# Kernel tuning notes

Hardware: AMD Instinct MI355X
Metric: run time of the kernel (lower is better)

Reference implementation:

```python
import jax, jax.numpy as jnp
import numpy as np

B, N, E = 16, 2048, 1024
G, V = 2, 320
D = E // G
TAU = 2.0


def setup_inputs() -> dict:
    key = jax.random.key(0)
    k1, k2, k3, k4 = jax.random.split(key, 4)
    x = jax.random.normal(k1, (B, N, E), dtype=jnp.float32)
    u = jax.random.uniform(k2, (B, N, G, V), dtype=jnp.float32)
    W = jax.random.normal(k3, (E, G * V), dtype=jnp.float32) * 0.02
    b = jnp.zeros((G * V,), dtype=jnp.float32)
    codebook = jax.random.normal(k4, (G, V, D), dtype=jnp.float32)
    return {"x": x, "u": u, "W": W, "b": b, "codebook": codebook}


def reference(x, u, W, b, codebook):
    Bx, Nx, Ex = x.shape
    Gx, Vx, Dx = codebook.shape
    # linear projection -> per-group logits [B,N,G,V]
    h = (jnp.einsum('bne,ef->bnf', x, W) + b).reshape(Bx, Nx, Gx, Vx)
    # gumbel noise from uniform samples (clamped away from 0/1)
    eps = 1e-7
    g = -jnp.log(-jnp.log(u * (1.0 - 2.0 * eps) + eps))
    soft = jax.nn.softmax((h + g) / TAU, axis=-1)
    # hard one-hot with straight-through estimator (matches torch hard=True)
    idx = jnp.argmax(soft, axis=-1)
    hard = jax.nn.one_hot(idx, Vx, dtype=soft.dtype)
    y = hard - jax.lax.stop_gradient(soft) + soft  # [B,N,G,V]
    # select code vectors: equivalent to broadcast-mul + sum over V
    code_vector = jnp.einsum('bngv,gvd->bngd', y, codebook).reshape(Bx, Nx, Gx * Dx)
    # codebook usage entropy: sum one-hots over time, softmax over V per group
    p = jax.nn.softmax(jnp.sum(y, axis=1), axis=-1)  # [B,G,V]
    entropy = -jnp.sum(p * jnp.log(p + 1e-8)) / (Gx * Vx)
    return code_vector, entropy
```

## Files before the change

kernel.cpp:

```cpp
#include <hip/hip_runtime.h>

namespace {

constexpr int Bsz = 16, Nsz = 2048, Esz = 1024, Gsz = 2, Vsz = 320, Dsz = 512;
constexpr int Msz = Bsz * Nsz;
constexpr int Fsz = Gsz * Vsz;
constexpr int BM = 128, BN = 128, BK = 32;
constexpr int NKC = Esz / 32;

typedef __attribute__((ext_vector_type(8))) short bf16x8;
typedef __attribute__((ext_vector_type(4))) float f32x4;
typedef unsigned int u32;
typedef unsigned short u16;

__device__ __forceinline__ void load_lds16(const void* g, void* l) {
  __builtin_amdgcn_global_load_lds(
      (const __attribute__((address_space(1))) u32*)g,
      (__attribute__((address_space(3))) u32*)l, 16, 0, 0);
}

__device__ __forceinline__ ushort f2bf(float f) {
  union { float f; unsigned u; } v; v.f = f;
  unsigned r = (v.u + 0x7FFFu + ((v.u >> 16) & 1u)) >> 16;
  return (ushort)r;
}
__device__ __forceinline__ float bf2f(ushort h) {
  union { unsigned u; float f; } v; v.u = ((unsigned)h) << 16;
  return v.f;
}

__device__ __forceinline__ float gumb_precise(float uu) {
  const float C0 = 1.0f - 2.0f * 1e-7f;
  float up = uu * C0;
  up = up + 1e-7f;
  return -logf(-logf(up));
}
__device__ __forceinline__ float gumb_fast(float uu) {
  const float C0 = 1.0f - 2.0f * 1e-7f;
  const float up = fmaf(uu, C0, 1e-7f);
  const float d = 1.0f - up;
  const float ypoly =
      d * fmaf(d, fmaf(d, fmaf(d, fmaf(d, 0.2f, 0.25f), 0.33333334f), 0.5f), 1.0f);
  const float yfast = -__logf(up);
  const float y = (up >= 0.84f) ? ypoly : yfast;
  return -__logf(y);
}

struct Top2 { float v1, v2; int i1, i2; };
__device__ __forceinline__ void t2_feed(Top2& t, float z, int f) {
  if (z > t.v1 || (z == t.v1 && f < t.i1)) {
    t.v2 = t.v1; t.i2 = t.i1; t.v1 = z; t.i1 = f;
  } else if (z > t.v2 || (z == t.v2 && f < t.i2)) {
    t.v2 = z; t.i2 = f;
  }
}
__device__ __forceinline__ void t2_merge(Top2& t, float ov1, int oi1, float ov2,
                                         int oi2) {
  if (ov1 > t.v1 || (ov1 == t.v1 && oi1 < t.i1)) {
    const bool keep = (t.v1 > ov2) || (t.v1 == ov2 && t.i1 < oi2);
    t.v2 = keep ? t.v1 : ov2; t.i2 = keep ? t.i1 : oi2;
    t.v1 = ov1; t.i1 = oi1;
  } else if (ov1 > t.v2 || (ov1 == t.v2 && oi1 < t.i2)) {
    t.v2 = ov1; t.i2 = oi1;
  }
}

__device__ __forceinline__ uint2 pack_hi_trunc(float4 a) {
  uint2 r;
  r.x = (__float_as_uint(a.x) >> 16) | (__float_as_uint(a.y) & 0xffff0000u);
  r.y = (__float_as_uint(a.z) >> 16) | (__float_as_uint(a.w) & 0xffff0000u);
  return r;
}
__device__ __forceinline__ float4 resid_trunc(float4 a) {
  float4 r;
  r.x = a.x - __uint_as_float(__float_as_uint(a.x) & 0xffff0000u);
  r.y = a.y - __uint_as_float(__float_as_uint(a.y) & 0xffff0000u);
  r.z = a.z - __uint_as_float(__float_as_uint(a.z) & 0xffff0000u);
  r.w = a.w - __uint_as_float(__float_as_uint(a.w) & 0xffff0000u);
  return r;
}


__global__ __launch_bounds__(256) void k_prep(const float* __restrict__ W,
                                              u16* __restrict__ wt) {
  const int tid = threadIdx.x;
  const int l = tid & 63;
  const int blob = blockIdx.x * 4 + (tid >> 6);
  const int fb = blob >> 5, kc = blob & 31;
  const int f = fb * 16 + (l & 15);
  const int k0 = kc * 32 + (l >> 4) * 8;
  ushort hh[8], ll[8];
#pragma unroll
  for (int j = 0; j < 8; ++j) {
    const float v = W[(size_t)(k0 + j) * Fsz + f];
    hh[j] = f2bf(v);
    ll[j] = f2bf(v - bf2f(hh[j]));
  }
  uint4 qh, ql;
  qh.x = hh[0] | ((u32)hh[1] << 16); qh.y = hh[2] | ((u32)hh[3] << 16);
  qh.z = hh[4] | ((u32)hh[5] << 16); qh.w = hh[6] | ((u32)hh[7] << 16);
  ql.x = ll[0] | ((u32)ll[1] << 16); ql.y = ll[2] | ((u32)ll[3] << 16);
  ql.z = ll[4] | ((u32)ll[5] << 16); ql.w = ll[6] | ((u32)ll[7] << 16);
  *(uint4*)(wt + ((size_t)blob * 2 + 0) * 512 + l * 8) = qh;
  *(uint4*)(wt + ((size_t)blob * 2 + 1) * 512 + l * 8) = ql;
}

__global__ __launch_bounds__(256) void k_prepx(const float* __restrict__ x,
                                               u16* __restrict__ xt) {
  const int tid = threadIdx.x;
  const int l = tid & 63;
  const int blob = blockIdx.x * 4 + (tid >> 6);
  const int mb = blob >> 5, kc = blob & 31;
  const size_t row = (size_t)mb * 16 + (l & 15);
  const int k0 = kc * 32 + (l >> 4) * 8;
  const float4 a0 = *(const float4*)(x + row * Esz + k0);
  const float4 a1 = *(const float4*)(x + row * Esz + k0 + 4);
  const uint2 h0 = pack_hi_trunc(a0), h1 = pack_hi_trunc(a1);
  const uint2 l0 = pack_hi_trunc(resid_trunc(a0));
  const uint2 l1 = pack_hi_trunc(resid_trunc(a1));
  uint4 qh, ql;
  qh.x = h0.x; qh.y = h0.y; qh.z = h1.x; qh.w = h1.y;
  ql.x = l0.x; ql.y = l0.y; ql.z = l1.x; ql.w = l1.y;
  *(uint4*)(xt + ((size_t)blob * 2 + 0) * 512 + l * 8) = qh;
  *(uint4*)(xt + ((size_t)blob * 2 + 1) * 512 + l * 8) = ql;
}

__global__ __launch_bounds__(256, 4) void k_gemm(
    const float* __restrict__ u, const float* __restrict__ bias,
    const u16* __restrict__ xt, const u16* __restrict__ wt,
    float4* __restrict__ partial) {
  __shared__ __align__(16) u16 sm[12288];
  u16* As = sm;
  u16* Bs = sm + 8192;

  const int tid = threadIdx.x;
  const int bid = blockIdx.x;
  const int tile = (bid & 7) * 320 + (bid >> 3);
  const int mt = tile / 10, nt = tile - mt * 10;
  const int m0 = mt * BM;
  const int n0 = nt * 64;

  const int lane = tid & 63, w = tid >> 6;
  const int lrow = lane & 15, quad = lane >> 4;

  f32x4 acc[2][4];
#pragma unroll
  for (int i = 0; i < 2; ++i)
#pragma unroll
    for (int j = 0; j < 4; ++j) acc[i][j] = (f32x4){0.f, 0.f, 0.f, 0.f};

  const u16* src0[6];
  u16* dst0[6];
#pragma unroll
  for (int i = 0; i < 6; ++i) {
    const int cc = w + 4 * i;
    const int isA = (cc < 16) ? 1 : 0;
    const int c = isA ? cc : (cc - 16);
    const int gb = (isA ? (m0 >> 4) : (n0 >> 4)) + (c >> 1);
    const int p = c & 1;
    src0[i] = (isA ? xt : wt) + ((size_t)gb * NKC * 2 + p) * 512 + lane * 8;
    dst0[i] = (isA ? As : Bs) + c * 512;
  }

#pragma unroll
  for (int i = 0; i < 6; ++i) load_lds16(src0[i], dst0[i]);

  for (int kc = 0; kc < NKC; ++kc) {
    __syncthreads();
    bf16x8 ah[2], al[2], bh[4], bl[4];
#pragma unroll
    for (int rt = 0; rt < 2; ++rt) {
      const int blk = w * 2 + rt;
      ah[rt] = *(const bf16x8*)(As + (blk * 2 + 0) * 512 + lane * 8);
      al[rt] = *(const bf16x8*)(As + (blk * 2 + 1) * 512 + lane * 8);
    }
#pragma unroll
    for (int ct = 0; ct < 4; ++ct) {
      bh[ct] = *(const bf16x8*)(Bs + (ct * 2 + 0) * 512 + lane * 8);
      bl[ct] = *(const bf16x8*)(Bs + (ct * 2 + 1) * 512 + lane * 8);
    }
    __syncthreads();
    if (kc + 1 < NKC) {
      const size_t off = (size_t)(kc + 1) * 1024;
#pragma unroll
      for (int i = 0; i < 6; ++i) load_lds16(src0[i] + off, dst0[i]);
    }
    __builtin_amdgcn_sched_barrier(0);
#pragma unroll
    for (int ct = 0; ct < 4; ++ct)
#pragma unroll
      for (int rt = 0; rt < 2; ++rt) {
        acc[rt][ct] = __builtin_amdgcn_mfma_f32_16x16x32_bf16(al[rt], bh[ct], acc[rt][ct], 0, 0, 0);
        acc[rt][ct] = __builtin_amdgcn_mfma_f32_16x16x32_bf16(ah[rt], bl[ct], acc[rt][ct], 0, 0, 0);
        acc[rt][ct] = __builtin_amdgcn_mfma_f32_16x16x32_bf16(ah[rt], bh[ct], acc[rt][ct], 0, 0, 0);
      }
  }

  const int pcol = nt;
#pragma unroll
  for (int rt = 0; rt < 2; ++rt) {
#pragma unroll
    for (int rg = 0; rg < 4; ++rg) {
      const int row = w * 32 + rt * 16 + quad * 4 + rg;
      const size_t m = (size_t)(m0 + row);
      Top2 t; t.v1 = -3.4e38f; t.v2 = -3.4e38f; t.i1 = 1 << 30; t.i2 = 1 << 30;
#pragma unroll
      for (int ct = 0; ct < 4; ++ct) {
        const int f = n0 + ct * 16 + lrow;
        const float z = acc[rt][ct][rg] + bias[f] + gumb_fast(u[m * 640 + f]);
        t2_feed(t, z, f);
      }
#pragma unroll
      for (int off = 1; off < 16; off <<= 1) {
        const float ov1 = __shfl_xor(t.v1, off, 16);
        const int oi1 = __shfl_xor(t.i1, off, 16);
        const float ov2 = __shfl_xor(t.v2, off, 16);
        const int oi2 = __shfl_xor(t.i2, off, 16);
        t2_merge(t, ov1, oi1, ov2, oi2);
      }
      if (lrow == 0) {
        float4 o;
        o.x = t.v1; o.y = __int_as_float(t.i1);
        o.z = t.v2; o.w = __int_as_float(t.i2);
        partial[m * 10 + pcol] = o;
      }
    }
  }
}

__global__ __launch_bounds__(256) void k_select(
    const float4* __restrict__ partial, const float* __restrict__ x,
    const float* __restrict__ W, const float* __restrict__ bias,
    const float* __restrict__ u, int2* __restrict__ idx_out,
    int* __restrict__ counts) {
  const int tid = threadIdx.x;
  const size_t m = (size_t)blockIdx.x * 256 + tid;
  int vsel[2];
#pragma unroll
  for (int g = 0; g < 2; ++g) {
    Top2 t; t.v1 = -3.4e38f; t.v2 = -3.4e38f; t.i1 = 1 << 30; t.i2 = 1 << 30;
#pragma unroll
    for (int p = 0; p < 5; ++p) {
      const float4 q = partial[m * 10 + g * 5 + p];
      t2_merge(t, q.x, __float_as_int(q.y), q.z, __float_as_int(q.w));
    }
    int i1 = t.i1;
    if (t.v1 - t.v2 < 1e-3f) {
      const int i2 = t.i2;
      const float* xp = x + m * Esz;
      float h1 = 0.f, h2 = 0.f;
      for (int k = 0; k < Esz; ++k) {
        const float xv = xp[k];
        h1 = fmaf(xv, W[(size_t)k * Fsz + i1], h1);
        h2 = fmaf(xv, W[(size_t)k * Fsz + i2], h2);
      }
      const float z1 = h1 + bias[i1] + gumb_precise(u[m * 640 + i1]);
      const float z2 = h2 + bias[i2] + gumb_precise(u[m * 640 + i2]);
      if (z2 > z1 || (z2 == z1 && i2 < i1)) i1 = i2;
    }
    const int v = i1 - g * Vsz;
    vsel[g] = v;
    const int b = (int)(m >> 11);
    atomicAdd(&counts[(b * Gsz + g) * Vsz + v], 1);
  }
  int2 r; r.x = vsel[0]; r.y = vsel[1];
  idx_out[m] = r;
}

__global__ __launch_bounds__(256) void k_gather(const int2* __restrict__ idx,
                                                const float* __restrict__ cb,
                                                float* __restrict__ out) {
  __shared__ int2 sidx[32];
  const int tid = threadIdx.x;
  const size_t mbase = (size_t)blockIdx.x * 32;
  if (tid < 32) sidx[tid] = idx[mbase + tid];
  __syncthreads();
  const int gq = tid >> 7, dq = tid & 127;
  for (int it = 0; it < 32; ++it) {
    const int2 p = sidx[it];
    const int v = gq ? p.y : p.x;
    const float4 cv =
        *(const float4*)(cb + ((size_t)(gq * Vsz + v)) * Dsz + dq * 4);
    *(float4*)(out + (mbase + it) * (size_t)(Gsz * Dsz) + tid * 4) = cv;
  }
}


__global__ __launch_bounds__(256) void k_prep_fb(const float* __restrict__ W,
                                                 u16* __restrict__ wt_h,
                                                 u16* __restrict__ wt_l) {
  const int f = blockIdx.x;
  const int k0 = threadIdx.x * 4;
  float v[4];
#pragma unroll
  for (int i = 0; i < 4; ++i) v[i] = W[(size_t)(k0 + i) * Fsz + f];
  ushort4 hh, ll;
  hh.x = f2bf(v[0]); ll.x = f2bf(v[0] - bf2f(hh.x));
  hh.y = f2bf(v[1]); ll.y = f2bf(v[1] - bf2f(hh.y));
  hh.z = f2bf(v[2]); ll.z = f2bf(v[2] - bf2f(hh.z));
  hh.w = f2bf(v[3]); ll.w = f2bf(v[3] - bf2f(hh.w));
  *(ushort4*)(wt_h + (size_t)f * Esz + k0) = hh;
  *(ushort4*)(wt_l + (size_t)f * Esz + k0) = ll;
}

__global__ __launch_bounds__(256) void k_gemm_fb(
    const float* __restrict__ x, const float* __restrict__ u,
    const float* __restrict__ bias, const u16* __restrict__ wth,
    const u16* __restrict__ wtl, float4* __restrict__ partial) {
  __shared__ __align__(16) u16 sm[16384];
  u16* xs_h = sm;
  u16* xs_l = sm + 4096;
  u16* bs_h = sm + 8192;
  u16* bs_l = sm + 12288;

  const int tid = threadIdx.x;
  const int n0 = blockIdx.x * BN;
  const int m0 = blockIdx.y * BM;
  const int lane = tid & 63, w = tid >> 6;
  const int wr = w >> 1, wc = w & 1;
  const int lrow = lane & 15, quad = lane >> 4;

  f32x4 acc[4][4];
#pragma unroll
  for (int i = 0; i < 4; ++i)
#pragma unroll
    for (int j = 0; j < 4; ++j) acc[i][j] = (f32x4){0.f, 0.f, 0.f, 0.f};

  for (int k0 = 0; k0 < Esz; k0 += BK) {
    float4 av[4];
#pragma unroll
    for (int s = 0; s < 4; ++s) {
      const int id = tid + 256 * s;
      const int row = id >> 3, kq = id & 7;
      av[s] = *(const float4*)(x + (size_t)(m0 + row) * Esz + k0 + kq * 4);
    }
    __syncthreads();
#pragma unroll
    for (int c = 0; c < 4; ++c) {
      const int chunk = w + 4 * c;
      const int plane = chunk >> 3, ch = chunk & 7;
      const u16* src = (plane ? wtl : wth) +
                       (size_t)(n0 + ch * 16 + (lane >> 2)) * Esz + k0 +
                       (lane & 3) * 8;
      u16* dst = (plane ? bs_l : bs_h) + ch * 512;
      load_lds16(src, dst);
    }
#pragma unroll
    for (int s = 0; s < 4; ++s) {
      const int id = tid + 256 * s;
      const int row = id >> 3, kq = id & 7;
      const u32 u0 = __float_as_uint(av[s].x), u1 = __float_as_uint(av[s].y);
      const u32 u2 = __float_as_uint(av[s].z), u3 = __float_as_uint(av[s].w);
      uint2 hh, ll;
      hh.x = (u0 >> 16) | (u1 & 0xffff0000u);
      hh.y = (u2 >> 16) | (u3 & 0xffff0000u);
      const float r0 = av[s].x - __uint_as_float(u0 & 0xffff0000u);
      const float r1 = av[s].y - __uint_as_float(u1 & 0xffff0000u);
      const float r2 = av[s].z - __uint_as_float(u2 & 0xffff0000u);
      const float r3 = av[s].w - __uint_as_float(u3 & 0xffff0000u);
      ll.x = (__float_as_uint(r0) >> 16) | (__float_as_uint(r1) & 0xffff0000u);
      ll.y = (__float_as_uint(r2) >> 16) | (__float_as_uint(r3) & 0xffff0000u);
      *(uint2*)(xs_h + row * 32 + kq * 4) = hh;
      *(uint2*)(xs_l + row * 32 + kq * 4) = ll;
    }
    __syncthreads();

    bf16x8 ah[4], al[4];
#pragma unroll
    for (int rt = 0; rt < 4; ++rt) {
      const int off = (wr * 64 + rt * 16 + lrow) * 32 + quad * 8;
      ah[rt] = *(const bf16x8*)(xs_h + off);
      al[rt] = *(const bf16x8*)(xs_l + off);
    }
#pragma unroll
    for (int ct = 0; ct < 4; ++ct) {
      const int off = (wc * 64 + ct * 16 + lrow) * 32 + quad * 8;
      const bf16x8 bh = *(const bf16x8*)(bs_h + off);
      const bf16x8 bl = *(const bf16x8*)(bs_l + off);
#pragma unroll
      for (int rt = 0; rt < 4; ++rt) {
        acc[rt][ct] = __builtin_amdgcn_mfma_f32_16x16x32_bf16(al[rt], bh, acc[rt][ct], 0, 0, 0);
        acc[rt][ct] = __builtin_amdgcn_mfma_f32_16x16x32_bf16(ah[rt], bl, acc[rt][ct], 0, 0, 0);
        acc[rt][ct] = __builtin_amdgcn_mfma_f32_16x16x32_bf16(ah[rt], bh, acc[rt][ct], 0, 0, 0);
      }
    }
  }

  const int pcol = blockIdx.x * 2 + wc;
#pragma unroll
  for (int rt = 0; rt < 4; ++rt) {
#pragma unroll
    for (int rg = 0; rg < 4; ++rg) {
      const int row = wr * 64 + rt * 16 + quad * 4 + rg;
      const size_t m = (size_t)(m0 + row);
      Top2 t; t.v1 = -3.4e38f; t.v2 = -3.4e38f; t.i1 = 1 << 30; t.i2 = 1 << 30;
#pragma unroll
      for (int ct = 0; ct < 4; ++ct) {
        const int f = n0 + wc * 64 + ct * 16 + lrow;
        const float z = acc[rt][ct][rg] + bias[f] + gumb_fast(u[m * 640 + f]);
        t2_feed(t, z, f);
      }
#pragma unroll
      for (int off = 1; off < 16; off <<= 1) {
        const float ov1 = __shfl_xor(t.v1, off, 16);
        const int oi1 = __shfl_xor(t.i1, off, 16);
        const float ov2 = __shfl_xor(t.v2, off, 16);
        const int oi2 = __shfl_xor(t.i2, off, 16);
        t2_merge(t, ov1, oi1, ov2, oi2);
      }
      if (lrow == 0) {
        float4 o;
        o.x = t.v1; o.y = __int_as_float(t.i1);
        o.z = t.v2; o.w = __int_as_float(t.i2);
        partial[m * 10 + pcol] = o;
      }
    }
  }
}

__global__ __launch_bounds__(256) void k_select_fb(
    const float4* __restrict__ partial, const float* __restrict__ x,
    const float* __restrict__ W, const float* __restrict__ bias,
    const float* __restrict__ u, const float* __restrict__ cb,
    float* __restrict__ out, int* __restrict__ counts) {
  __shared__ int idx_sh[256][2];
  const int tid = threadIdx.x;
  const size_t m = (size_t)blockIdx.x * 256 + tid;

#pragma unroll
  for (int g = 0; g < 2; ++g) {
    Top2 t; t.v1 = -3.4e38f; t.v2 = -3.4e38f; t.i1 = 1 << 30; t.i2 = 1 << 30;
#pragma unroll
    for (int p = 0; p < 5; ++p) {
      const float4 q = partial[m * 10 + g * 5 + p];
      t2_merge(t, q.x, __float_as_int(q.y), q.z, __float_as_int(q.w));
    }
    int i1 = t.i1;
    if (t.v1 - t.v2 < 1e-3f) {
      const int i2 = t.i2;
      const float* xp = x + m * Esz;
      float h1 = 0.f, h2 = 0.f;
      for (int k = 0; k < Esz; ++k) {
        const float xv = xp[k];
        h1 = fmaf(xv, W[(size_t)k * Fsz + i1], h1);
        h2 = fmaf(xv, W[(size_t)k * Fsz + i2], h2);
      }
      const float z1 = h1 + bias[i1] + gumb_precise(u[m * 640 + i1]);
      const float z2 = h2 + bias[i2] + gumb_precise(u[m * 640 + i2]);
      if (z2 > z1 || (z2 == z1 && i2 < i1)) i1 = i2;
    }
    const int v = i1 - g * Vsz;
    idx_sh[tid][g] = v;
    const int b = (int)(m >> 11);
    atomicAdd(&counts[(b * Gsz + g) * Vsz + v], 1);
  }
  __syncthreads();

  const size_t mbase = (size_t)blockIdx.x * 256;
  const int gq = tid >> 7, dq = tid & 127;
  for (int it = 0; it < 256; ++it) {
    const int v = idx_sh[it][gq];
    const float4 cv =
        *(const float4*)(cb + ((size_t)(gq * Vsz + v)) * Dsz + dq * 4);
    *(float4*)(out + (mbase + it) * (size_t)(Gsz * Dsz) + tid * 4) = cv;
  }
}

__global__ __launch_bounds__(64) void k_entropy(const int* __restrict__ counts,
                                                float* __restrict__ partial) {
  const int bg = blockIdx.x;
  const int lane = threadIdx.x;
  float c[5];
  float mx = -3.4e38f;
#pragma unroll
  for (int t = 0; t < 5; ++t) {
    c[t] = (float)counts[bg * Vsz + lane + 64 * t];
    mx = fmaxf(mx, c[t]);
  }
#pragma unroll
  for (int off = 32; off; off >>= 1) mx = fmaxf(mx, __shfl_xor(mx, off));
  float e[5];
  float s = 0.f;
#pragma unroll
  for (int t = 0; t < 5; ++t) {
    e[t] = expf(c[t] - mx);
    s += e[t];
  }
#pragma unroll
  for (int off = 32; off; off >>= 1) s += __shfl_xor(s, off);
  float ent = 0.f;
#pragma unroll
  for (int t = 0; t < 5; ++t) {
    const float p = e[t] / s;
    ent += p * logf(p + 1e-8f);
  }
#pragma unroll
  for (int off = 32; off; off >>= 1) ent += __shfl_xor(ent, off);
  if (lane == 0) partial[bg] = ent;
}

__global__ __launch_bounds__(64) void k_final(const float* __restrict__ partial,
                                              float* __restrict__ dst) {
  const int lane = threadIdx.x;
  float v = (lane < 32) ? partial[lane] : 0.f;
#pragma unroll
  for (int off = 32; off; off >>= 1) v += __shfl_xor(v, off);
  if (lane == 0) dst[0] = -v / (float)(Gsz * Vsz);
}

}

extern "C" void kernel_launch(void* const* d_in, const int* in_sizes, int n_in,
                              void* d_out, int out_size, void* d_ws,
                              size_t ws_size, hipStream_t stream) {
  const float* x = (const float*)d_in[0];
  const float* u = (const float*)d_in[1];
  const float* W = (const float*)d_in[2];
  const float* bias = (const float*)d_in[3];
  const float* cb = (const float*)d_in[4];
  float* out = (float*)d_out;

  int* counts = (int*)d_ws;
  float* epart = (float*)((char*)d_ws + 40960);
  float4* partial = (float4*)((char*)d_ws + 65536);
  const size_t PART_END = 65536 + (size_t)Msz * 10 * 16;
  const size_t NEED_NEW = PART_END + 262144 + 2621440 + (size_t)Msz * Esz * 4;

  hipMemsetAsync(d_ws, 0, 40960, stream);

  if (ws_size >= NEED_NEW) {
    int2* idx = (int2*)((char*)d_ws + PART_END);
    u16* wt = (u16*)((char*)d_ws + PART_END + 262144);
    u16* xt = (u16*)((char*)d_ws + PART_END + 262144 + 2621440);
    k_prep<<<320, 256, 0, stream>>>(W, wt);
    k_prepx<<<16384, 256, 0, stream>>>(x, xt);
    k_gemm<<<(Msz / BM) * 10, 256, 0, stream>>>(u, bias, xt, wt, partial);
    k_select<<<Msz / 256, 256, 0, stream>>>(partial, x, W, bias, u, idx,
                                            counts);
    k_gather<<<Msz / 32, 256, 0, stream>>>(idx, cb, out);
  } else {
    u16* wth = (u16*)((char*)d_ws + PART_END);
    u16* wtl = wth + (size_t)Fsz * Esz;
    k_prep_fb<<<Fsz, 256, 0, stream>>>(W, wth, wtl);
    k_gemm_fb<<<dim3(Fsz / BN, Msz / BM), 256, 0, stream>>>(x, u, bias, wth,
                                                            wtl, partial);
    k_select_fb<<<Msz / 256, 256, 0, stream>>>(partial, x, W, bias, u, cb, out,
                                               counts);
  }
  k_entropy<<<Bsz * Gsz, 64, 0, stream>>>(counts, epart);
  k_final<<<1, 64, 0, stream>>>(epart, out + (size_t)Msz * Esz);
}
```

Before: 638.2 us.

## Double-buffer GEMM LDS staging, transpose W for rescoring, shrink gather blocks

The GEMM kernel now keeps two LDS buffers and issues the global-to-LDS loads two k-steps ahead. It waits with explicit vmcnt/lgkmcnt counters instead of two full __syncthreads per iteration, so load latency can overlap the MFMA work, at the cost of doubling LDS use and lowering the occupancy hint from 4 to 3. The prep kernel also writes a transposed fp32 copy of W, which lets the near-tie rescoring in k_select read contiguous float4 rows instead of strided columns. k_gather now handles 8 rows per block and reads indices straight from global memory instead of staging them in shared memory.

```diff
diff --git a/kernel.cpp b/kernel.cpp
--- a/kernel.cpp
+++ b/kernel.cpp
@@ -82,19 +82,21 @@
 
 
 __global__ __launch_bounds__(256) void k_prep(const float* __restrict__ W,
-                                              u16* __restrict__ wt) {
+                                              u16* __restrict__ wt,
+                                              float* __restrict__ wtT) {
   const int tid = threadIdx.x;
   const int l = tid & 63;
   const int blob = blockIdx.x * 4 + (tid >> 6);
   const int fb = blob >> 5, kc = blob & 31;
   const int f = fb * 16 + (l & 15);
   const int k0 = kc * 32 + (l >> 4) * 8;
+  float v[8];
   ushort hh[8], ll[8];
 #pragma unroll
   for (int j = 0; j < 8; ++j) {
-    const float v = W[(size_t)(k0 + j) * Fsz + f];
-    hh[j] = f2bf(v);
-    ll[j] = f2bf(v - bf2f(hh[j]));
+    v[j] = W[(size_t)(k0 + j) * Fsz + f];
+    hh[j] = f2bf(v[j]);
+    ll[j] = f2bf(v[j] - bf2f(hh[j]));
   }
   uint4 qh, ql;
   qh.x = hh[0] | ((u32)hh[1] << 16); qh.y = hh[2] | ((u32)hh[3] << 16);
@@ -103,6 +105,11 @@
   ql.z = ll[4] | ((u32)ll[5] << 16); ql.w = ll[6] | ((u32)ll[7] << 16);
   *(uint4*)(wt + ((size_t)blob * 2 + 0) * 512 + l * 8) = qh;
   *(uint4*)(wt + ((size_t)blob * 2 + 1) * 512 + l * 8) = ql;
+  float4 t0, t1;
+  t0.x = v[0]; t0.y = v[1]; t0.z = v[2]; t0.w = v[3];
+  t1.x = v[4]; t1.y = v[5]; t1.z = v[6]; t1.w = v[7];
+  *(float4*)(wtT + (size_t)f * Esz + k0) = t0;
+  *(float4*)(wtT + (size_t)f * Esz + k0 + 4) = t1;
 }
 
 __global__ __launch_bounds__(256) void k_prepx(const float* __restrict__ x,
@@ -125,13 +132,11 @@
   *(uint4*)(xt + ((size_t)blob * 2 + 1) * 512 + l * 8) = ql;
 }
 
-__global__ __launch_bounds__(256, 4) void k_gemm(
+__global__ __launch_bounds__(256, 3) void k_gemm(
     const float* __restrict__ u, const float* __restrict__ bias,
     const u16* __restrict__ xt, const u16* __restrict__ wt,
     float4* __restrict__ partial) {
-  __shared__ __align__(16) u16 sm[12288];
-  u16* As = sm;
-  u16* Bs = sm + 8192;
+  __shared__ __align__(16) u16 sm[24576];
 
   const int tid = threadIdx.x;
   const int bid = blockIdx.x;
@@ -150,7 +155,7 @@
     for (int j = 0; j < 4; ++j) acc[i][j] = (f32x4){0.f, 0.f, 0.f, 0.f};
 
   const u16* src0[6];
-  u16* dst0[6];
+  int dstoff[6];
 #pragma unroll
   for (int i = 0; i < 6; ++i) {
     const int cc = w + 4 * i;
@@ -159,14 +164,30 @@
     const int gb = (isA ? (m0 >> 4) : (n0 >> 4)) + (c >> 1);
     const int p = c & 1;
     src0[i] = (isA ? xt : wt) + ((size_t)gb * NKC * 2 + p) * 512 + lane * 8;
-    dst0[i] = (isA ? As : Bs) + c * 512;
-  }
-
-#pragma unroll
-  for (int i = 0; i < 6; ++i) load_lds16(src0[i], dst0[i]);
+    dstoff[i] = (isA ? 0 : 8192) + c * 512;
+  }
+
+  auto stage = [&](int buf, int kc) {
+    const size_t go = (size_t)kc * 1024;
+#pragma unroll
+    for (int i = 0; i < 6; ++i)
+      load_lds16(src0[i] + go, sm + buf * 12288 + dstoff[i]);
+  };
+
+  stage(0, 0);
+  stage(1, 1);
+  int cur = 0;
 
   for (int kc = 0; kc < NKC; ++kc) {
-    __syncthreads();
+    if (kc < NKC - 1) {
+      asm volatile("s_waitcnt vmcnt(6)" ::: "memory");
+    } else {
+      asm volatile("s_waitcnt vmcnt(0)" ::: "memory");
+    }
+    __builtin_amdgcn_s_barrier();
+
+    const u16* As = sm + cur * 12288;
+    const u16* Bs = As + 8192;
     bf16x8 ah[2], al[2], bh[4], bl[4];
 #pragma unroll
     for (int rt = 0; rt < 2; ++rt) {
@@ -179,12 +200,10 @@
       bh[ct] = *(const bf16x8*)(Bs + (ct * 2 + 0) * 512 + lane * 8);
       bl[ct] = *(const bf16x8*)(Bs + (ct * 2 + 1) * 512 + lane * 8);
     }
-    __syncthreads();
-    if (kc + 1 < NKC) {
-      const size_t off = (size_t)(kc + 1) * 1024;
-#pragma unroll
-      for (int i = 0; i < 6; ++i) load_lds16(src0[i] + off, dst0[i]);
-    }
+    asm volatile("s_waitcnt lgkmcnt(0)" ::: "memory");
+    __builtin_amdgcn_sched_barrier(0);
+    __builtin_amdgcn_s_barrier();
+    if (kc + 2 < NKC) stage(cur, kc + 2);
     __builtin_amdgcn_sched_barrier(0);
 #pragma unroll
     for (int ct = 0; ct < 4; ++ct)
@@ -194,6 +213,7 @@
         acc[rt][ct] = __builtin_amdgcn_mfma_f32_16x16x32_bf16(ah[rt], bl[ct], acc[rt][ct], 0, 0, 0);
         acc[rt][ct] = __builtin_amdgcn_mfma_f32_16x16x32_bf16(ah[rt], bh[ct], acc[rt][ct], 0, 0, 0);
       }
+    cur ^= 1;
   }
 
   const int pcol = nt;
@@ -230,7 +250,7 @@
 
 __global__ __launch_bounds__(256) void k_select(
     const float4* __restrict__ partial, const float* __restrict__ x,
-    const float* __restrict__ W, const float* __restrict__ bias,
+    const float* __restrict__ wtT, const float* __restrict__ bias,
     const float* __restrict__ u, int2* __restrict__ idx_out,
     int* __restrict__ counts) {
   const int tid = threadIdx.x;
@@ -248,11 +268,17 @@
     if (t.v1 - t.v2 < 1e-3f) {
       const int i2 = t.i2;
       const float* xp = x + m * Esz;
+      const float* w1 = wtT + (size_t)i1 * Esz;
+      const float* w2 = wtT + (size_t)i2 * Esz;
       float h1 = 0.f, h2 = 0.f;
-      for (int k = 0; k < Esz; ++k) {
-        const float xv = xp[k];
-        h1 = fmaf(xv, W[(size_t)k * Fsz + i1], h1);
-        h2 = fmaf(xv, W[(size_t)k * Fsz + i2], h2);
+      for (int k = 0; k < Esz; k += 4) {
+        const float4 xv = *(const float4*)(xp + k);
+        const float4 a = *(const float4*)(w1 + k);
+        const float4 b = *(const float4*)(w2 + k);
+        h1 = fmaf(xv.x, a.x, h1); h1 = fmaf(xv.y, a.y, h1);
+        h1 = fmaf(xv.z, a.z, h1); h1 = fmaf(xv.w, a.w, h1);
+        h2 = fmaf(xv.x, b.x, h2); h2 = fmaf(xv.y, b.y, h2);
+        h2 = fmaf(xv.z, b.z, h2); h2 = fmaf(xv.w, b.w, h2);
       }
       const float z1 = h1 + bias[i1] + gumb_precise(u[m * 640 + i1]);
       const float z2 = h2 + bias[i2] + gumb_precise(u[m * 640 + i2]);
@@ -270,14 +296,12 @@
 __global__ __launch_bounds__(256) void k_gather(const int2* __restrict__ idx,
                                                 const float* __restrict__ cb,
                                                 float* __restrict__ out) {
-  __shared__ int2 sidx[32];
-  const int tid = threadIdx.x;
-  const size_t mbase = (size_t)blockIdx.x * 32;
-  if (tid < 32) sidx[tid] = idx[mbase + tid];
-  __syncthreads();
+  const int tid = threadIdx.x;
+  const size_t mbase = (size_t)blockIdx.x * 8;
   const int gq = tid >> 7, dq = tid & 127;
-  for (int it = 0; it < 32; ++it) {
-    const int2 p = sidx[it];
+#pragma unroll
+  for (int it = 0; it < 8; ++it) {
+    const int2 p = idx[mbase + it];
     const int v = gq ? p.y : p.x;
     const float4 cv =
         *(const float4*)(cb + ((size_t)(gq * Vsz + v)) * Dsz + dq * 4);
@@ -524,20 +548,22 @@
   float* epart = (float*)((char*)d_ws + 40960);
   float4* partial = (float4*)((char*)d_ws + 65536);
   const size_t PART_END = 65536 + (size_t)Msz * 10 * 16;
-  const size_t NEED_NEW = PART_END + 262144 + 2621440 + (size_t)Msz * Esz * 4;
+  const size_t NEED_NEW =
+      PART_END + 262144 + 2621440 + 2621440 + (size_t)Msz * Esz * 4;
 
   hipMemsetAsync(d_ws, 0, 40960, stream);
 
   if (ws_size >= NEED_NEW) {
     int2* idx = (int2*)((char*)d_ws + PART_END);
     u16* wt = (u16*)((char*)d_ws + PART_END + 262144);
-    u16* xt = (u16*)((char*)d_ws + PART_END + 262144 + 2621440);
-    k_prep<<<320, 256, 0, stream>>>(W, wt);
+    float* wtT = (float*)((char*)d_ws + PART_END + 262144 + 2621440);
+    u16* xt = (u16*)((char*)d_ws + PART_END + 262144 + 2621440 + 2621440);
+    k_prep<<<320, 256, 0, stream>>>(W, wt, wtT);
     k_prepx<<<16384, 256, 0, stream>>>(x, xt);
     k_gemm<<<(Msz / BM) * 10, 256, 0, stream>>>(u, bias, xt, wt, partial);
-    k_select<<<Msz / 256, 256, 0, stream>>>(partial, x, W, bias, u, idx,
+    k_select<<<Msz / 256, 256, 0, stream>>>(partial, x, wtT, bias, u, idx,
                                             counts);
-    k_gather<<<Msz / 32, 256, 0, stream>>>(idx, cb, out);
+    k_gather<<<Msz / 8, 256, 0, stream>>>(idx, cb, out);
   } else {
     u16* wth = (u16*)((char*)d_ws + PART_END);
     u16* wtl = wth + (size_t)Fsz * Esz;
```

New measurement: 540.0 us. -15.4%, faster.
